# Performance work log

Hardware: AMD Instinct MI355X
Metric: run time of the kernel (lower is better)

Reference implementation:

```python
import jax, jax.numpy as jnp
import numpy as np

N_USERS = 100000
N_ITEMS = 30000
E = 1000000
D = 128
N_LAYERS = 3
W_SELF = 1.0
W_SEEK = 0.5


def _graph_conv(x_src, src, dst, n_src, n_dst, edge_weight=None):
    """DGL GraphConv(weight=False, bias=False, norm='both'):
    out = D_dst^{-1/2} A (D_src^{-1/2} x), edge_weight multiplies messages."""
    ones = jnp.ones(src.shape[0], dtype=x_src.dtype)
    deg_s = jax.ops.segment_sum(ones, src, num_segments=n_src)
    deg_d = jax.ops.segment_sum(ones, dst, num_segments=n_dst)
    norm_s = jnp.where(deg_s > 0, jax.lax.rsqrt(jnp.maximum(deg_s, 1.0)), 0.0)
    norm_d = jnp.where(deg_d > 0, jax.lax.rsqrt(jnp.maximum(deg_d, 1.0)), 0.0)
    m = (x_src * norm_s[:, None])[src]  # [E, D] gather
    if edge_weight is not None:
        m = m * edge_weight[:, None]
    agg = jax.ops.segment_sum(m, dst, num_segments=n_dst)  # [n_dst, D] scatter-add
    return agg * norm_d[:, None]


def setup_inputs() -> dict:
    key = jax.random.key(0)
    ks = jax.random.split(key, 9)
    return {
        'user_emb': jax.random.normal(ks[0], (N_USERS, D), jnp.float32),
        'item_emb': jax.random.normal(ks[1], (N_ITEMS, D), jnp.float32),
        'weight_edge': jax.random.uniform(ks[2], (E,), jnp.float32),
        'ori_u': jax.random.randint(ks[3], (E,), 0, N_USERS, jnp.int32),
        'ori_i': jax.random.randint(ks[4], (E,), 0, N_ITEMS, jnp.int32),
        'seek_u': jax.random.randint(ks[5], (E,), 0, N_USERS, jnp.int32),
        'seek_i': jax.random.randint(ks[6], (E,), 0, N_ITEMS, jnp.int32),
        'dn_u': jax.random.randint(ks[7], (E,), 0, N_USERS, jnp.int32),
        'dn_i': jax.random.randint(ks[8], (E,), 0, N_ITEMS, jnp.int32),
    }


def reference(user_emb, item_emb, weight_edge, ori_u, ori_i, seek_u, seek_i, dn_u, dn_i):
    # ----- first branch: original graph + seek graph fusion -----
    hu, hi = user_emb, item_emb
    for _ in range(N_LAYERS):
        h_user = _graph_conv(hi, ori_i, ori_u, N_ITEMS, N_USERS)
        h_item = _graph_conv(hu, ori_u, ori_i, N_USERS, N_ITEMS)
        h_user_seek = _graph_conv(hi, seek_i, seek_u, N_ITEMS, N_USERS, weight_edge)
        h_item_seek = _graph_conv(hu, seek_u, seek_i, N_USERS, N_ITEMS)
        hu = h_user * W_SELF + h_user_seek * W_SEEK
        hi = h_item * W_SELF + h_item_seek * W_SEEK
    # h_sub1 is an alias of h in the original code (same dict object).
    # ----- second branch: dn graph, seek terms computed from FINAL h (constant per iter) -----
    h_user_seek_f = _graph_conv(hi, seek_i, seek_u, N_ITEMS, N_USERS, weight_edge)
    h_item_seek_f = _graph_conv(hu, seek_u, seek_i, N_USERS, N_ITEMS)
    h1u, h1i = user_emb, item_emb
    for _ in range(N_LAYERS):
        h_user_dn = _graph_conv(h1i, dn_i, dn_u, N_ITEMS, N_USERS)
        h_item_dn = _graph_conv(h1u, dn_u, dn_i, N_USERS, N_ITEMS)
        h1u = h_user_dn * W_SELF + h_user_seek_f * W_SEEK
        h1i = h_item_dn * W_SELF + h_item_seek_f * W_SEEK
    # (h, h_sub1, h1) with h_sub1 == h
    return (hu, hi, hu, hi, h1u, h1i)
```

## Files before the change

kernel.cpp:

```cpp
#include <hip/hip_runtime.h>

#define N_USERS 100000
#define N_ITEMS 30000
#define NE      1000000
#define D       128
#define CHUNK   4096
#define HCHUNK  8192
#define STAGE_B 7424
#define SH_U    9
#define SH_I    7
#define NB_U    ((N_USERS + (1 << SH_U) - 1) >> SH_U)
#define NB_I    ((N_ITEMS + (1 << SH_I) - 1) >> SH_I)

__device__ __forceinline__ unsigned f2bf(float f) {
    unsigned u = __float_as_uint(f);
    return (u + 0x7fffu + ((u >> 16) & 1u)) >> 16;
}
__device__ __forceinline__ float bflo(unsigned v) { return __uint_as_float(v << 16); }
__device__ __forceinline__ float bfhi(unsigned v) { return __uint_as_float(v & 0xffff0000u); }

struct HistArgs { const int* dst[6]; int shift[6]; int* bh; };

__global__ __launch_bounds__(256) void k_bhist(HistArgs a) {
    __shared__ int h[256];
    const int l = blockIdx.y;
    const int* __restrict__ dst = a.dst[l];
    const int sh = a.shift[l];
    const int t = threadIdx.x;
    h[t] = 0;
    __syncthreads();
    const int e0 = blockIdx.x * HCHUNK;
    const int e1 = min(e0 + HCHUNK, NE);
    for (int e = e0 + t; e < e1; e += 256) atomicAdd(&h[dst[e] >> sh], 1);
    __syncthreads();
    if (h[t]) atomicAdd(&a.bh[l * 256 + t], h[t]);
}

__global__ void k_scanB(const int* __restrict__ bh, int* __restrict__ bstart,
                        int* __restrict__ gcur) {
    __shared__ int lds[256];
    const int l = blockIdx.x, t = threadIdx.x;
    const int x = bh[l * 256 + t];
    lds[t] = x;
    __syncthreads();
    for (int o = 1; o < 256; o <<= 1) {
        int add = (t >= o) ? lds[t - o] : 0;
        __syncthreads();
        lds[t] += add;
        __syncthreads();
    }
    const int excl = lds[t] - x;
    bstart[l * 257 + t] = excl;
    gcur[l * 256 + t] = excl;
    if (t == 255) bstart[l * 257 + 256] = lds[t];
}

struct BinList { const int* dst; const int* srcp; const float* w; int shift; int* gcur; int2* tmp; };
struct BinArgs { BinList l[6]; };

__global__ __launch_bounds__(256) void k_binA(BinArgs ba) {
    const BinList L = ba.l[blockIdx.y];
    __shared__ int2 stg[CHUNK];
    __shared__ unsigned char bkt[CHUNK];
    __shared__ int hist[256], sbase[256], scur[256], gbase[256];
    const int t = threadIdx.x;
    const int e0 = blockIdx.x * CHUNK;
    const int ccnt = min(CHUNK, NE - e0);
    hist[t] = 0;
    __syncthreads();
#pragma unroll
    for (int j = 0; j < CHUNK / 256; ++j) {
        const int e = e0 + j * 256 + t;
        if (e < NE) atomicAdd(&hist[L.dst[e] >> L.shift], 1);
    }
    __syncthreads();
    {
        const int x = hist[t];
        sbase[t] = x;
        __syncthreads();
        for (int o = 1; o < 256; o <<= 1) {
            int add = (t >= o) ? sbase[t - o] : 0;
            __syncthreads();
            sbase[t] += add;
            __syncthreads();
        }
        const int excl = sbase[t] - x;
        __syncthreads();
        sbase[t] = excl;
        scur[t] = excl;
        gbase[t] = (x > 0) ? atomicAdd(&L.gcur[t], x) : 0;
    }
    __syncthreads();
#pragma unroll
    for (int j = 0; j < CHUNK / 256; ++j) {
        const int e = e0 + j * 256 + t;
        if (e < NE) {
            const int d = L.dst[e], s = L.srcp[e];
            const int b = d >> L.shift;
            const int p = atomicAdd(&scur[b], 1);
            stg[p] = make_int2(((d & ((1 << L.shift) - 1)) << 17) | s,
                               L.w ? __float_as_int(L.w[e]) : 0);
            bkt[p] = (unsigned char)b;
        }
    }
    __syncthreads();
    for (int i = t; i < ccnt; i += 256) {
        const int b = bkt[i];
        L.tmp[gbase[b] + (i - sbase[b])] = stg[i];
    }
}

struct DegArgs {
    const int2* tmp[6];
    const int* bstart;
    int* rs[6];
    float* rdeg[6];
    int shift[6]; int n[6]; int bofs[7];
};

__global__ __launch_bounds__(256) void k_bdeg(DegArgs a) {
    __shared__ int cnt[512];
    __shared__ int lds[256];
    int l = 0;
    while ((int)blockIdx.x >= a.bofs[l + 1]) ++l;
    const int b = blockIdx.x - a.bofs[l];
    const int sh = a.shift[l], n = a.n[l];
    const int node0 = b << sh;
    const int node1 = min(node0 + (1 << sh), n);
    const int nn = node1 - node0;
    const int bs = a.bstart[l * 257 + b], be = a.bstart[l * 257 + b + 1];
    const int t = threadIdx.x;
    cnt[t] = 0; cnt[t + 256] = 0;
    __syncthreads();
    const int2* __restrict__ tmp = a.tmp[l];
    for (int i = bs + t; i < be; i += 256) atomicAdd(&cnt[((unsigned)tmp[i].x) >> 17], 1);
    __syncthreads();
    const int c0 = cnt[2 * t], c1 = cnt[2 * t + 1];
    lds[t] = c0 + c1;
    __syncthreads();
    for (int o = 1; o < 256; o <<= 1) {
        int add = (t >= o) ? lds[t - o] : 0;
        __syncthreads();
        lds[t] += add;
        __syncthreads();
    }
    const int ep = lds[t] - (c0 + c1);
    int* __restrict__ rs = a.rs[l];
    float* __restrict__ rd = a.rdeg[l];
    if (2 * t < nn) {
        rs[node0 + 2 * t] = bs + ep;
        rd[node0 + 2 * t] = rsqrtf((float)max(c0, 1));
    }
    if (2 * t + 1 < nn) {
        rs[node0 + 2 * t + 1] = bs + ep + c0;
        rd[node0 + 2 * t + 1] = rsqrtf((float)max(c1, 1));
    }
    if (t == 0) rs[node1] = be;
}

struct SortArgs {
    const int2* tmp[6]; int2* outp[6];
    const int* rs[6];
    const float* rdD[6]; const float* rdS[6];
    const int* bstart;
    int shift[6]; int n[6]; int mode[6];
    int bofs[7];
};

__global__ __launch_bounds__(256) void k_binB(SortArgs a) {
    __shared__ int2 stg[STAGE_B];
    __shared__ int lcur[512];
    __shared__ float rdl[512];
    int l = 0;
    while ((int)blockIdx.x >= a.bofs[l + 1]) ++l;
    const int b = blockIdx.x - a.bofs[l];
    const int sh = a.shift[l], n = a.n[l], mode = a.mode[l];
    const int node0 = b << sh;
    const int node1 = min(node0 + (1 << sh), n);
    const int nn = node1 - node0;
    const int bs = a.bstart[l * 257 + b], be = a.bstart[l * 257 + b + 1], cnt = be - bs;
    const int t = threadIdx.x;
    const int* __restrict__ rs = a.rs[l];
    const float* __restrict__ rdD = a.rdD[l];
    for (int k = t; k < nn; k += 256) {
        lcur[k] = rs[node0 + k] - bs;
        rdl[k] = rdD[node0 + k];
    }
    __syncthreads();
    const int2* __restrict__ tmp = a.tmp[l];
    int2* __restrict__ outp = a.outp[l];
    const float* __restrict__ rdS = a.rdS[l];
    if (cnt <= STAGE_B) {
        for (int i = bs + t; i < be; i += 256) {
            const int2 v = tmp[i];
            const int dl = ((unsigned)v.x) >> 17, src = v.x & 0x1FFFF;
            float c = rdl[dl] * rdS[src];
            if (mode == 1) c *= 0.5f * __int_as_float(v.y);
            else if (mode == 2) c *= 0.5f;
            const int slot = atomicAdd(&lcur[dl], 1);
            stg[slot] = make_int2(src << 8, __float_as_int(c));
        }
        __syncthreads();
        for (int i = t; i < cnt; i += 256) outp[bs + i] = stg[i];
    } else {
        for (int i = bs + t; i < be; i += 256) {
            const int2 v = tmp[i];
            const int dl = ((unsigned)v.x) >> 17, src = v.x & 0x1FFFF;
            float c = rdl[dl] * rdS[src];
            if (mode == 1) c *= 0.5f * __int_as_float(v.y);
            else if (mode == 2) c *= 0.5f;
            const int slot = atomicAdd(&lcur[dl], 1);
            outp[bs + slot] = make_int2(src << 8, __float_as_int(c));
        }
    }
}

__global__ void k_tobf16(const float* __restrict__ in, ushort* __restrict__ out, int n4) {
    int i = blockIdx.x * blockDim.x + threadIdx.x;
    if (i >= n4) return;
    float4 v = ((const float4*)in)[i];
    ((uint2*)out)[i] = make_uint2((f2bf(v.y) << 16) | f2bf(v.x),
                                  (f2bf(v.w) << 16) | f2bf(v.z));
}

struct ConvSide {
    const ushort* x;
    const int*  rs1; const int2* p1;
    const int*  rs2; const int2* p2;
    const ushort* base;
    float*  outf; float* outf2;
    ushort* outb;
    int n;
};

__device__ __forceinline__ void accum_list(const char* __restrict__ xb,
                                           const int* __restrict__ rs,
                                           const int2* __restrict__ p,
                                           int row, int laneb,
                                           float& ax, float& ay) {
    const int j0 = rs[row], j1 = rs[row + 1];
    const int lane = laneb >> 2;
    for (int jb = j0; jb < j1; jb += 64) {
        int2 mp = make_int2(0, 0);
        if (jb + lane < j1) mp = p[jb + lane];
        const int cnt = min(64, j1 - jb);
        int t = 0;
        for (; t + 8 <= cnt; t += 8) {
            unsigned v[8]; float c[8];
#pragma unroll
            for (int k = 0; k < 8; ++k) {
                const int so = __builtin_amdgcn_readlane(mp.x, t + k);
                c[k] = __int_as_float(__builtin_amdgcn_readlane(mp.y, t + k));
                v[k] = *(const unsigned*)(xb + so + laneb);
            }
#pragma unroll
            for (int k = 0; k < 8; ++k) {
                ax = fmaf(c[k], bflo(v[k]), ax);
                ay = fmaf(c[k], bfhi(v[k]), ay);
            }
        }
        if (t + 4 <= cnt) {
            unsigned v[4]; float c[4];
#pragma unroll
            for (int k = 0; k < 4; ++k) {
                const int so = __builtin_amdgcn_readlane(mp.x, t + k);
                c[k] = __int_as_float(__builtin_amdgcn_readlane(mp.y, t + k));
                v[k] = *(const unsigned*)(xb + so + laneb);
            }
#pragma unroll
            for (int k = 0; k < 4; ++k) {
                ax = fmaf(c[k], bflo(v[k]), ax);
                ay = fmaf(c[k], bfhi(v[k]), ay);
            }
            t += 4;
        }
        for (; t < cnt; ++t) {
            const int so = __builtin_amdgcn_readlane(mp.x, t);
            const float c = __int_as_float(__builtin_amdgcn_readlane(mp.y, t));
            const unsigned v = *(const unsigned*)(xb + so + laneb);
            ax = fmaf(c, bflo(v), ax);
            ay = fmaf(c, bfhi(v), ay);
        }
    }
}

__global__ void k_conv1(ConvSide S) {
    const int q = (int)gridDim.x >> 3;
    const int bid = (int)blockIdx.x;
    const int rb = (bid & 7) * q + (bid >> 3);
    int row = rb * 4 + (int)(threadIdx.x >> 6);
    const int lane = threadIdx.x & 63;
    if (row >= S.n) return;
    row = __builtin_amdgcn_readfirstlane(row);
    const int laneb = lane << 2;
    const size_t roff = (size_t)row * D + lane * 2;
    float ax = 0.f, ay = 0.f;
    if (S.base) {
        const unsigned b = *(const unsigned*)(S.base + roff);
        ax = bflo(b); ay = bfhi(b);
    }
    const char* xb = (const char*)S.x;
    accum_list(xb, S.rs1, S.p1, row, laneb, ax, ay);
    if (S.rs2) accum_list(xb, S.rs2, S.p2, row, laneb, ax, ay);
    if (S.outf)  *(float2*)(S.outf  + roff) = make_float2(ax, ay);
    if (S.outf2) *(float2*)(S.outf2 + roff) = make_float2(ax, ay);
    if (S.outb)  *(unsigned*)(S.outb + roff) = (f2bf(ay) << 16) | f2bf(ax);
}

extern "C" void kernel_launch(void* const* d_in, const int* in_sizes, int n_in,
                              void* d_out, int out_size, void* d_ws, size_t ws_size,
                              hipStream_t stream) {
    const float* user_emb = (const float*)d_in[0];
    const float* item_emb = (const float*)d_in[1];
    const float* w_edge   = (const float*)d_in[2];
    const int* ou = (const int*)d_in[3];
    const int* oi = (const int*)d_in[4];
    const int* su = (const int*)d_in[5];
    const int* si = (const int*)d_in[6];
    const int* du = (const int*)d_in[7];
    const int* di = (const int*)d_in[8];
    float* out = (float*)d_out;

    const size_t SZ_U = (size_t)N_USERS * D;
    const size_t SZ_I = (size_t)N_ITEMS * D;

    float* o0 = out;
    float* o1 = o0 + SZ_U;
    float* o2 = o1 + SZ_I;
    float* o3 = o2 + SZ_U;
    float* o4 = o3 + SZ_I;
    float* o5 = o4 + SZ_U;

    ushort* tU0 = (ushort*)o4;  ushort* tU1 = tU0 + SZ_U;
    ushort* tI0 = (ushort*)o5;  ushort* tI1 = tI0 + SZ_I;

    char* ws = (char*)d_ws;
    size_t off = 0;
    auto alloc = [&](size_t bytes) -> void* {
        void* p = ws + off;
        off = (off + bytes + 255) & ~(size_t)255;
        return p;
    };

    int* rOU = (int*)alloc((N_USERS + 1) * 4);
    int* rOI = (int*)alloc((N_ITEMS + 1) * 4);
    int* rSU = (int*)alloc((N_USERS + 1) * 4);
    int* rSI = (int*)alloc((N_ITEMS + 1) * 4);
    int* rDU = (int*)alloc((N_USERS + 1) * 4);
    int* rDI = (int*)alloc((N_ITEMS + 1) * 4);

    float* rdOU = (float*)alloc(N_USERS * 4);
    float* rdOI = (float*)alloc(N_ITEMS * 4);
    float* rdSU = (float*)alloc(N_USERS * 4);
    float* rdSI = (float*)alloc(N_ITEMS * 4);
    float* rdDU = (float*)alloc(N_USERS * 4);
    float* rdDI = (float*)alloc(N_ITEMS * 4);

    size_t bhBegin = off;
    int* bh     = (int*)alloc(6 * 256 * 4);
    size_t bhEnd = off;
    int* bstart = (int*)alloc(6 * 257 * 4);
    int* gcur   = (int*)alloc(6 * 256 * 4);

    int2* pOU = (int2*)alloc((size_t)NE * 8);
    int2* pOI = (int2*)alloc((size_t)NE * 8);
    int2* pSU = (int2*)alloc((size_t)NE * 8);
    int2* pSI = (int2*)alloc((size_t)NE * 8);
    int2* pDU = (int2*)alloc((size_t)NE * 8);
    int2* pDI = (int2*)alloc((size_t)NE * 8);

    int2* qOU = (int2*)alloc((size_t)NE * 8);
    int2* qOI = (int2*)alloc((size_t)NE * 8);
    int2* qSU = (int2*)alloc((size_t)NE * 8);
    int2* qSI = (int2*)alloc((size_t)NE * 8);
    int2* qDU = (int2*)alloc((size_t)NE * 8);
    int2* qDI = (int2*)alloc((size_t)NE * 8);

    ushort* ebU = (ushort*)alloc(SZ_U * 2);
    ushort* ebI = (ushort*)alloc(SZ_I * 2);
    ushort* fUb = (ushort*)alloc(SZ_U * 2);
    ushort* fIb = (ushort*)alloc(SZ_I * 2);

    hipMemsetAsync(ws + bhBegin, 0, bhEnd - bhBegin, stream);
    hipLaunchKernelGGL(k_tobf16, dim3((unsigned)(SZ_U / 4 + 255) / 256), dim3(256), 0, stream,
                       user_emb, ebU, (int)(SZ_U / 4));
    hipLaunchKernelGGL(k_tobf16, dim3((unsigned)(SZ_I / 4 + 255) / 256), dim3(256), 0, stream,
                       item_emb, ebI, (int)(SZ_I / 4));

    HistArgs ha;
    ha.dst[0] = ou; ha.shift[0] = SH_U;
    ha.dst[1] = oi; ha.shift[1] = SH_I;
    ha.dst[2] = su; ha.shift[2] = SH_U;
    ha.dst[3] = si; ha.shift[3] = SH_I;
    ha.dst[4] = du; ha.shift[4] = SH_U;
    ha.dst[5] = di; ha.shift[5] = SH_I;
    ha.bh = bh;
    hipLaunchKernelGGL(k_bhist, dim3((NE + HCHUNK - 1) / HCHUNK, 6), dim3(256), 0, stream, ha);
    hipLaunchKernelGGL(k_scanB, dim3(6), dim3(256), 0, stream, bh, bstart, gcur);

    BinArgs ba;
    ba.l[0] = { ou, oi, nullptr, SH_U, gcur + 0 * 256, qOU };
    ba.l[1] = { oi, ou, nullptr, SH_I, gcur + 1 * 256, qOI };
    ba.l[2] = { su, si, w_edge,  SH_U, gcur + 2 * 256, qSU };
    ba.l[3] = { si, su, nullptr, SH_I, gcur + 3 * 256, qSI };
    ba.l[4] = { du, di, nullptr, SH_U, gcur + 4 * 256, qDU };
    ba.l[5] = { di, du, nullptr, SH_I, gcur + 5 * 256, qDI };
    hipLaunchKernelGGL(k_binA, dim3((NE + CHUNK - 1) / CHUNK, 6), dim3(256), 0, stream, ba);

    int bofs[7];
    {
        int nb[6] = { NB_U, NB_I, NB_U, NB_I, NB_U, NB_I };
        bofs[0] = 0;
        for (int i = 0; i < 6; ++i) bofs[i + 1] = bofs[i] + nb[i];
    }

    DegArgs da;
    da.tmp[0] = qOU; da.rs[0] = rOU; da.rdeg[0] = rdOU; da.shift[0] = SH_U; da.n[0] = N_USERS;
    da.tmp[1] = qOI; da.rs[1] = rOI; da.rdeg[1] = rdOI; da.shift[1] = SH_I; da.n[1] = N_ITEMS;
    da.tmp[2] = qSU; da.rs[2] = rSU; da.rdeg[2] = rdSU; da.shift[2] = SH_U; da.n[2] = N_USERS;
    da.tmp[3] = qSI; da.rs[3] = rSI; da.rdeg[3] = rdSI; da.shift[3] = SH_I; da.n[3] = N_ITEMS;
    da.tmp[4] = qDU; da.rs[4] = rDU; da.rdeg[4] = rdDU; da.shift[4] = SH_U; da.n[4] = N_USERS;
    da.tmp[5] = qDI; da.rs[5] = rDI; da.rdeg[5] = rdDI; da.shift[5] = SH_I; da.n[5] = N_ITEMS;
    da.bstart = bstart;
    for (int i = 0; i < 7; ++i) da.bofs[i] = bofs[i];
    hipLaunchKernelGGL(k_bdeg, dim3(bofs[6]), dim3(256), 0, stream, da);

    SortArgs so;
    so.tmp[0] = qOU; so.outp[0] = pOU; so.rs[0] = rOU; so.rdD[0] = rdOU; so.rdS[0] = rdOI;
    so.shift[0] = SH_U; so.n[0] = N_USERS; so.mode[0] = 0;
    so.tmp[1] = qOI; so.outp[1] = pOI; so.rs[1] = rOI; so.rdD[1] = rdOI; so.rdS[1] = rdOU;
    so.shift[1] = SH_I; so.n[1] = N_ITEMS; so.mode[1] = 0;
    so.tmp[2] = qSU; so.outp[2] = pSU; so.rs[2] = rSU; so.rdD[2] = rdSU; so.rdS[2] = rdSI;
    so.shift[2] = SH_U; so.n[2] = N_USERS; so.mode[2] = 1;
    so.tmp[3] = qSI; so.outp[3] = pSI; so.rs[3] = rSI; so.rdD[3] = rdSI; so.rdS[3] = rdSU;
    so.shift[3] = SH_I; so.n[3] = N_ITEMS; so.mode[3] = 2;
    so.tmp[4] = qDU; so.outp[4] = pDU; so.rs[4] = rDU; so.rdD[4] = rdDU; so.rdS[4] = rdDI;
    so.shift[4] = SH_U; so.n[4] = N_USERS; so.mode[4] = 0;
    so.tmp[5] = qDI; so.outp[5] = pDI; so.rs[5] = rDI; so.rdD[5] = rdDI; so.rdS[5] = rdDU;
    so.shift[5] = SH_I; so.n[5] = N_ITEMS; so.mode[5] = 0;
    so.bstart = bstart;
    for (int i = 0; i < 7; ++i) so.bofs[i] = bofs[i];
    hipLaunchKernelGGL(k_binB, dim3(bofs[6]), dim3(256), 0, stream, so);

    auto mkside = [](const ushort* x, const int* rs1, const int2* p1,
                     const int* rs2, const int2* p2, const ushort* base,
                     float* outf, float* outf2, ushort* outb, int n) {
        ConvSide s; s.x = x; s.rs1 = rs1; s.p1 = p1; s.rs2 = rs2; s.p2 = p2;
        s.base = base; s.outf = outf; s.outf2 = outf2; s.outb = outb; s.n = n;
        return s;
    };
    auto conv1 = [&](const ConvSide& S) {
        const int nb = (S.n + 3) / 4;
        const int nwg = (nb + 7) & ~7;
        hipLaunchKernelGGL(k_conv1, dim3((unsigned)nwg), dim3(256), 0, stream, S);
    };

    conv1(mkside(ebI, rOU, pOU, rSU, pSU, nullptr, nullptr, nullptr, tU0, N_USERS));
    conv1(mkside(ebU, rOI, pOI, rSI, pSI, nullptr, nullptr, nullptr, tI0, N_ITEMS));
    conv1(mkside(tI0, rOU, pOU, rSU, pSU, nullptr, nullptr, nullptr, tU1, N_USERS));
    conv1(mkside(tU0, rOI, pOI, rSI, pSI, nullptr, nullptr, nullptr, tI1, N_ITEMS));
    conv1(mkside(tI1, rOU, pOU, rSU, pSU, nullptr, o0, o2, tU0, N_USERS));
    conv1(mkside(tU1, rOI, pOI, rSI, pSI, nullptr, o1, o3, tI0, N_ITEMS));

    conv1(mkside(tI0, rSU, pSU, nullptr, nullptr, nullptr, nullptr, nullptr, fUb, N_USERS));
    conv1(mkside(tU0, rSI, pSI, nullptr, nullptr, nullptr, nullptr, nullptr, fIb, N_ITEMS));

    conv1(mkside(ebI, rDU, pDU, nullptr, nullptr, fUb, nullptr, nullptr, tU1, N_USERS));
    conv1(mkside(ebU, rDI, pDI, nullptr, nullptr, fIb, nullptr, nullptr, tI1, N_ITEMS));
    conv1(mkside(tI1, rDU, pDU, nullptr, nullptr, fUb, nullptr, nullptr, ebU, N_USERS));
    conv1(mkside(tU1, rDI, pDI, nullptr, nullptr, fIb, nullptr, nullptr, ebI, N_ITEMS));
    conv1(mkside(ebI, rDU, pDU, nullptr, nullptr, fUb, o4, nullptr, nullptr, N_USERS));
    conv1(mkside(ebU, rDI, pDI, nullptr, nullptr, fIb, o5, nullptr, nullptr, N_ITEMS));
}
```

Measured before the change: 835.9 us.

## Split convolution into feature-dimension slices with multiple rows per wavefront

Each graph convolution now runs as several launches, each covering one slice of the embedding columns (two 128-byte slices for users, four 64-byte slices for items). Within a wave, groups of 32 or 16 lanes each handle a separate destination row, and edge metadata is broadcast with shuffles instead of readlane. The aim is a smaller gathered working set per launch that fits better in cache, plus more rows in flight to hide gather latency. In exchange, the edge lists are re-read once per slice, each gather touches fewer bytes, and rows with different degrees inside one wave now diverge.

```diff
diff --git a/kernel.cpp b/kernel.cpp
--- a/kernel.cpp
+++ b/kernel.cpp
@@ -223,7 +223,7 @@
                                   (f2bf(v.w) << 16) | f2bf(v.z));
 }
 
-struct ConvSide {
+struct ConvSliceArgs {
     const ushort* x;
     const int*  rs1; const int2* p1;
     const int*  rs2; const int2* p2;
@@ -231,27 +231,32 @@
     float*  outf; float* outf2;
     ushort* outb;
     int n;
+    int slice_byte;
 };
 
-__device__ __forceinline__ void accum_list(const char* __restrict__ xb,
-                                           const int* __restrict__ rs,
-                                           const int2* __restrict__ p,
-                                           int row, int laneb,
-                                           float& ax, float& ay) {
+template<int LPR>
+__device__ __forceinline__ void accum_slice(const char* __restrict__ xs,
+                                            const int* __restrict__ rs,
+                                            const int2* __restrict__ p,
+                                            int row, int lane,
+                                            float& ax, float& ay) {
     const int j0 = rs[row], j1 = rs[row + 1];
-    const int lane = laneb >> 2;
-    for (int jb = j0; jb < j1; jb += 64) {
+    const int li = lane & (LPR - 1);
+    const int gb = lane - li;
+    const int lib = li * 4;
+    for (int jb = j0; jb < j1; jb += LPR) {
         int2 mp = make_int2(0, 0);
-        if (jb + lane < j1) mp = p[jb + lane];
-        const int cnt = min(64, j1 - jb);
+        if (jb + li < j1) mp = p[jb + li];
+        const int cnt = min(LPR, j1 - jb);
         int t = 0;
         for (; t + 8 <= cnt; t += 8) {
             unsigned v[8]; float c[8];
 #pragma unroll
             for (int k = 0; k < 8; ++k) {
-                const int so = __builtin_amdgcn_readlane(mp.x, t + k);
-                c[k] = __int_as_float(__builtin_amdgcn_readlane(mp.y, t + k));
-                v[k] = *(const unsigned*)(xb + so + laneb);
+                const int sl = gb + t + k;
+                const int so = __shfl(mp.x, sl, 64);
+                c[k] = __int_as_float(__shfl(mp.y, sl, 64));
+                v[k] = *(const unsigned*)(xs + so + lib);
             }
 #pragma unroll
             for (int k = 0; k < 8; ++k) {
@@ -263,9 +268,10 @@
             unsigned v[4]; float c[4];
 #pragma unroll
             for (int k = 0; k < 4; ++k) {
-                const int so = __builtin_amdgcn_readlane(mp.x, t + k);
-                c[k] = __int_as_float(__builtin_amdgcn_readlane(mp.y, t + k));
-                v[k] = *(const unsigned*)(xb + so + laneb);
+                const int sl = gb + t + k;
+                const int so = __shfl(mp.x, sl, 64);
+                c[k] = __int_as_float(__shfl(mp.y, sl, 64));
+                v[k] = *(const unsigned*)(xs + so + lib);
             }
 #pragma unroll
             for (int k = 0; k < 4; ++k) {
@@ -275,36 +281,40 @@
             t += 4;
         }
         for (; t < cnt; ++t) {
-            const int so = __builtin_amdgcn_readlane(mp.x, t);
-            const float c = __int_as_float(__builtin_amdgcn_readlane(mp.y, t));
-            const unsigned v = *(const unsigned*)(xb + so + laneb);
+            const int sl = gb + t;
+            const int so = __shfl(mp.x, sl, 64);
+            const float c = __int_as_float(__shfl(mp.y, sl, 64));
+            const unsigned v = *(const unsigned*)(xs + so + lib);
             ax = fmaf(c, bflo(v), ax);
             ay = fmaf(c, bfhi(v), ay);
         }
     }
 }
 
-__global__ void k_conv1(ConvSide S) {
+template<int LPR>
+__global__ __launch_bounds__(256) void k_convS(ConvSliceArgs A) {
+    constexpr int RPW = 64 / LPR;
     const int q = (int)gridDim.x >> 3;
     const int bid = (int)blockIdx.x;
     const int rb = (bid & 7) * q + (bid >> 3);
-    int row = rb * 4 + (int)(threadIdx.x >> 6);
+    const int wid = rb * 4 + (int)(threadIdx.x >> 6);
     const int lane = threadIdx.x & 63;
-    if (row >= S.n) return;
-    row = __builtin_amdgcn_readfirstlane(row);
-    const int laneb = lane << 2;
-    const size_t roff = (size_t)row * D + lane * 2;
+    const int g = lane / LPR;
+    const int row = wid * RPW + g;
+    if (row >= A.n) return;
+    const int li = lane & (LPR - 1);
+    const size_t roff = (size_t)row * D + (A.slice_byte >> 1) + li * 2;
     float ax = 0.f, ay = 0.f;
-    if (S.base) {
-        const unsigned b = *(const unsigned*)(S.base + roff);
+    if (A.base) {
+        const unsigned b = *(const unsigned*)(A.base + roff);
         ax = bflo(b); ay = bfhi(b);
     }
-    const char* xb = (const char*)S.x;
-    accum_list(xb, S.rs1, S.p1, row, laneb, ax, ay);
-    if (S.rs2) accum_list(xb, S.rs2, S.p2, row, laneb, ax, ay);
-    if (S.outf)  *(float2*)(S.outf  + roff) = make_float2(ax, ay);
-    if (S.outf2) *(float2*)(S.outf2 + roff) = make_float2(ax, ay);
-    if (S.outb)  *(unsigned*)(S.outb + roff) = (f2bf(ay) << 16) | f2bf(ax);
+    const char* xs = (const char*)A.x + A.slice_byte;
+    accum_slice<LPR>(xs, A.rs1, A.p1, row, lane, ax, ay);
+    if (A.rs2) accum_slice<LPR>(xs, A.rs2, A.p2, row, lane, ax, ay);
+    if (A.outf)  *(float2*)(A.outf  + roff) = make_float2(ax, ay);
+    if (A.outf2) *(float2*)(A.outf2 + roff) = make_float2(ax, ay);
+    if (A.outb)  *(unsigned*)(A.outb + roff) = (f2bf(ay) << 16) | f2bf(ax);
 }
 
 extern "C" void kernel_launch(void* const* d_in, const int* in_sizes, int n_in,
@@ -442,33 +452,45 @@
     for (int i = 0; i < 7; ++i) so.bofs[i] = bofs[i];
     hipLaunchKernelGGL(k_binB, dim3(bofs[6]), dim3(256), 0, stream, so);
 
-    auto mkside = [](const ushort* x, const int* rs1, const int2* p1,
+    auto convU = [&](const ushort* x, const int* rs1, const int2* p1,
                      const int* rs2, const int2* p2, const ushort* base,
-                     float* outf, float* outf2, ushort* outb, int n) {
-        ConvSide s; s.x = x; s.rs1 = rs1; s.p1 = p1; s.rs2 = rs2; s.p2 = p2;
-        s.base = base; s.outf = outf; s.outf2 = outf2; s.outb = outb; s.n = n;
-        return s;
+                     float* outf, float* outf2, ushort* outb) {
+        const int waves = (N_USERS + 1) / 2;
+        const int nwg = (((waves + 3) / 4) + 7) & ~7;
+        for (int s = 0; s < 2; ++s) {
+            ConvSliceArgs A{ x, rs1, p1, rs2, p2, base, outf, outf2, outb,
+                             N_USERS, s * 128 };
+            hipLaunchKernelGGL(HIP_KERNEL_NAME(k_convS<32>), dim3((unsigned)nwg),
+                               dim3(256), 0, stream, A);
+        }
     };
-    auto conv1 = [&](const ConvSide& S) {
-        const int nb = (S.n + 3) / 4;
-        const int nwg = (nb + 7) & ~7;
-        hipLaunchKernelGGL(k_conv1, dim3((unsigned)nwg), dim3(256), 0, stream, S);
+    auto convI = [&](const ushort* x, const int* rs1, const int2* p1,
+                     const int* rs2, const int2* p2, const ushort* base,
+                     float* outf, float* outf2, ushort* outb) {
+        const int waves = (N_ITEMS + 3) / 4;
+        const int nwg = (((waves + 3) / 4) + 7) & ~7;
+        for (int s = 0; s < 4; ++s) {
+            ConvSliceArgs A{ x, rs1, p1, rs2, p2, base, outf, outf2, outb,
+                             N_ITEMS, s * 64 };
+            hipLaunchKernelGGL(HIP_KERNEL_NAME(k_convS<16>), dim3((unsigned)nwg),
+                               dim3(256), 0, stream, A);
+        }
     };
 
-    conv1(mkside(ebI, rOU, pOU, rSU, pSU, nullptr, nullptr, nullptr, tU0, N_USERS));
-    conv1(mkside(ebU, rOI, pOI, rSI, pSI, nullptr, nullptr, nullptr, tI0, N_ITEMS));
-    conv1(mkside(tI0, rOU, pOU, rSU, pSU, nullptr, nullptr, nullptr, tU1, N_USERS));
-    conv1(mkside(tU0, rOI, pOI, rSI, pSI, nullptr, nullptr, nullptr, tI1, N_ITEMS));
-    conv1(mkside(tI1, rOU, pOU, rSU, pSU, nullptr, o0, o2, tU0, N_USERS));
-    conv1(mkside(tU1, rOI, pOI, rSI, pSI, nullptr, o1, o3, tI0, N_ITEMS));
-
-    conv1(mkside(tI0, rSU, pSU, nullptr, nullptr, nullptr, nullptr, nullptr, fUb, N_USERS));
-    conv1(mkside(tU0, rSI, pSI, nullptr, nullptr, nullptr, nullptr, nullptr, fIb, N_ITEMS));
-
-    conv1(mkside(ebI, rDU, pDU, nullptr, nullptr, fUb, nullptr, nullptr, tU1, N_USERS));
-    conv1(mkside(ebU, rDI, pDI, nullptr, nullptr, fIb, nullptr, nullptr, tI1, N_ITEMS));
-    conv1(mkside(tI1, rDU, pDU, nullptr, nullptr, fUb, nullptr, nullptr, ebU, N_USERS));
-    conv1(mkside(tU1, rDI, pDI, nullptr, nullptr, fIb, nullptr, nullptr, ebI, N_ITEMS));
-    conv1(mkside(ebI, rDU, pDU, nullptr, nullptr, fUb, o4, nullptr, nullptr, N_USERS));
-    conv1(mkside(ebU, rDI, pDI, nullptr, nullptr, fIb, o5, nullptr, nullptr, N_ITEMS));
-}
+    convU(ebI, rOU, pOU, rSU, pSU, nullptr, nullptr, nullptr, tU0);
+    convI(ebU, rOI, pOI, rSI, pSI, nullptr, nullptr, nullptr, tI0);
+    convU(tI0, rOU, pOU, rSU, pSU, nullptr, nullptr, nullptr, tU1);
+    convI(tU0, rOI, pOI, rSI, pSI, nullptr, nullptr, nullptr, tI1);
+    convU(tI1, rOU, pOU, rSU, pSU, nullptr, o0, o2, tU0);
+    convI(tU1, rOI, pOI, rSI, pSI, nullptr, o1, o3, tI0);
+
+    convU(tI0, rSU, pSU, nullptr, nullptr, nullptr, nullptr, nullptr, fUb);
+    convI(tU0, rSI, pSI, nullptr, nullptr, nullptr, nullptr, nullptr, fIb);
+
+    convU(ebI, rDU, pDU, nullptr, nullptr, fUb, nullptr, nullptr, tU1);
+    convI(ebU, rDI, pDI, nullptr, nullptr, fIb, nullptr, nullptr, tI1);
+    convU(tI1, rDU, pDU, nullptr, nullptr, fUb, nullptr, nullptr, ebU);
+    convI(tU1, rDI, pDI, nullptr, nullptr, fIb, nullptr, nullptr, ebI);
+    convU(ebI, rDU, pDU, nullptr, nullptr, fUb, o4, nullptr, nullptr);
+    convI(ebU, rDI, pDI, nullptr, nullptr, fIb, o5, nullptr, nullptr);
+}
```

Measured after the change: 1.353 ms. 61.9% more time.
